# Kernel optimization log

Measured on AMD Instinct MI355X. Metric: run time of the kernel, lower is better.

Reference implementation:

```python
import jax, jax.numpy as jnp
import numpy as np

BATCH, DIM, L, N = 2, 768, 2048, 16


def setup_inputs() -> dict:
    key = jax.random.key(0)
    ks = jax.random.split(key, 8)
    u = jax.random.normal(ks[0], (BATCH, DIM, L), dtype=jnp.float32)
    delta = jax.random.uniform(ks[1], (BATCH, DIM, L), dtype=jnp.float32)
    # A must be negative for a stable SSM (exp(delta*A) <= 1)
    A = -jax.random.uniform(ks[2], (DIM, N), dtype=jnp.float32, minval=0.5, maxval=1.5)
    B = jax.random.normal(ks[3], (BATCH, N, L), dtype=jnp.float32)
    C = jax.random.normal(ks[4], (BATCH, N, L), dtype=jnp.float32)
    D = jax.random.normal(ks[5], (DIM,), dtype=jnp.float32)
    z = jax.random.normal(ks[6], (BATCH, DIM, L), dtype=jnp.float32)
    delta_bias = 0.1 * jax.random.normal(ks[7], (DIM,), dtype=jnp.float32)
    return {"u": u, "delta": delta, "A": A, "B": B, "C": C,
            "D": D, "z": z, "delta_bias": delta_bias}


def _selective_scan(u, delta, A, B, C, D, z, delta_bias):
    # delta_softplus=True path of mamba_ssm selective_scan_fn
    delta = jax.nn.softplus(delta + delta_bias[None, :, None])  # (b, d, l)
    # discretize: deltaA = exp(delta * A), deltaB_u = delta * B * u
    deltaA = jnp.exp(jnp.einsum('bdl,dn->lbdn', delta, A))          # (l, b, d, n)
    deltaBu = jnp.einsum('bdl,bnl,bdl->lbdn', delta, B, u)          # (l, b, d, n)
    C_t = jnp.transpose(C, (2, 0, 1))                               # (l, b, n)

    def step(x, inp):
        a, bu, c = inp
        x = a * x + bu                                              # (b, d, n)
        y = jnp.einsum('bdn,bn->bd', x, c)                          # (b, d)
        return x, y

    x0 = jnp.zeros((BATCH, DIM, N), dtype=u.dtype)
    _, ys = jax.lax.scan(step, x0, (deltaA, deltaBu, C_t))          # ys: (l, b, d)
    y = jnp.transpose(ys, (1, 2, 0))                                # (b, d, l)
    out = y + u * D[None, :, None]
    out = out * jax.nn.silu(z)
    return out


def reference(u, delta, A, B, C, D, z, delta_bias):
    return _selective_scan(u, delta, A, B, C, D, z, delta_bias)
```

## Files before the change

kernel.cpp:

```cpp
#include <hip/hip_runtime.h>


#define LOG2E 1.4426950408889634f
#define LN2   0.6931471805599453f

constexpr int BATCH = 2, DIM = 768, L = 2048, N = 16;
constexpr int NC = 64, LC = 32;
static_assert(NC * LC == L, "chunking must cover L");

__device__ __forceinline__ float fexp2(float x) {
#if __has_builtin(__builtin_amdgcn_exp2f)
  return __builtin_amdgcn_exp2f(x);
#else
  return exp2f(x);
#endif
}

__device__ __forceinline__ float frcp(float x) {
#if __has_builtin(__builtin_amdgcn_rcpf)
  return __builtin_amdgcn_rcpf(x);
#else
  return 1.0f / x;
#endif
}

__device__ __forceinline__ float softplus(float v) {
  float s = LN2 * __log2f(1.0f + fexp2(v * LOG2E));
  return (v > 20.0f) ? v : s;
}

__device__ __forceinline__ float silu(float v) {
  float e = fexp2(-v * LOG2E);
  return v * frcp(1.0f + e);
}

__global__ __launch_bounds__(256) void k_transpose(
    const float* __restrict__ Bm, const float* __restrict__ Cm,
    float* __restrict__ Bt, float* __restrict__ Ct) {
  int g = blockIdx.x * 256 + threadIdx.x;
  int l = g % L, b = g / L;
#pragma unroll
  for (int n = 0; n < N; n++) {
    Bt[((long)b * L + l) * N + n] = Bm[((long)b * N + n) * L + l];
    Ct[((long)b * L + l) * N + n] = Cm[((long)b * N + n) * L + l];
  }
}

__global__ __launch_bounds__(64) void k_pass1(
    const float* __restrict__ u, const float* __restrict__ delta,
    const float* __restrict__ A, const float* __restrict__ dbias,
    const float* __restrict__ Bt, float* __restrict__ h, float* __restrict__ P) {
  int bi = blockIdx.x;
  int c = bi / 24;
  int r = bi % 24;
  int b = r / 12;
  int dg = r % 12;
  int d = dg * 64 + threadIdx.x;

  float A2[N];
#pragma unroll
  for (int n = 0; n < N; n++) A2[n] = A[d * N + n] * LOG2E;
  float bias = dbias[d];

  float x[N];
#pragma unroll
  for (int n = 0; n < N; n++) x[n] = 0.0f;
  float S = 0.0f;

  long base = ((long)(b * DIM + d)) * L + c * LC;
  const float* Brow = Bt + ((long)b * L + c * LC) * N;

  for (int half = 0; half < 2; ++half) {
    float dl[16], uu[16];
#pragma unroll
    for (int j4 = 0; j4 < 4; j4++) {
      float4 dv = *(const float4*)(delta + base + half * 16 + j4 * 4);
      float4 uv = *(const float4*)(u + base + half * 16 + j4 * 4);
      dl[j4 * 4 + 0] = dv.x; dl[j4 * 4 + 1] = dv.y; dl[j4 * 4 + 2] = dv.z; dl[j4 * 4 + 3] = dv.w;
      uu[j4 * 4 + 0] = uv.x; uu[j4 * 4 + 1] = uv.y; uu[j4 * 4 + 2] = uv.z; uu[j4 * 4 + 3] = uv.w;
    }
#pragma unroll
    for (int j = 0; j < 16; j++) {
      float sp = softplus(dl[j] + bias);
      S += sp;
      float du = sp * uu[j];
      const float* br = Brow + (half * 16 + j) * N;
#pragma unroll
      for (int n = 0; n < N; n++) {
        float a = fexp2(sp * A2[n]);
        x[n] = a * x[n] + du * br[n];
      }
    }
  }

  long hb = ((long)(b * DIM + d) * NC + c) * N;
#pragma unroll
  for (int n = 0; n < N; n++) {
    h[hb + n] = x[n];
    P[hb + n] = fexp2(S * A2[n]);
  }
}

__global__ __launch_bounds__(256) void k_pass2(float* __restrict__ h, const float* __restrict__ P) {
  int t = blockIdx.x * 256 + threadIdx.x;
  int n = t % N;
  int bd = t / N;
  long base = (long)bd * NC * N + n;
  float x = 0.0f;
#pragma unroll 8
  for (int c = 0; c < NC; c++) {
    long i = base + (long)c * N;
    float Pc = P[i];
    float hc = h[i];
    h[i] = x;
    x = Pc * x + hc;
  }
}

__global__ __launch_bounds__(64) void k_pass3(
    const float* __restrict__ u, const float* __restrict__ delta,
    const float* __restrict__ A, const float* __restrict__ dbias,
    const float* __restrict__ Bt, const float* __restrict__ Ct,
    const float* __restrict__ Dv, const float* __restrict__ z,
    const float* __restrict__ xinit, float* __restrict__ out) {
  int bi = blockIdx.x;
  int c = bi / 24;
  int r = bi % 24;
  int b = r / 12;
  int dg = r % 12;
  int d = dg * 64 + threadIdx.x;

  float A2[N];
#pragma unroll
  for (int n = 0; n < N; n++) A2[n] = A[d * N + n] * LOG2E;
  float bias = dbias[d];
  float Dd = Dv[d];

  long hb = ((long)(b * DIM + d) * NC + c) * N;
  float x[N];
#pragma unroll
  for (int n = 0; n < N; n++) x[n] = xinit[hb + n];

  long base = ((long)(b * DIM + d)) * L + c * LC;
  const float* Brow = Bt + ((long)b * L + c * LC) * N;
  const float* Crow = Ct + ((long)b * L + c * LC) * N;

  for (int half = 0; half < 2; ++half) {
    float dl[16], uu[16], y[16];
#pragma unroll
    for (int j4 = 0; j4 < 4; j4++) {
      float4 dv = *(const float4*)(delta + base + half * 16 + j4 * 4);
      float4 uv = *(const float4*)(u + base + half * 16 + j4 * 4);
      dl[j4 * 4 + 0] = dv.x; dl[j4 * 4 + 1] = dv.y; dl[j4 * 4 + 2] = dv.z; dl[j4 * 4 + 3] = dv.w;
      uu[j4 * 4 + 0] = uv.x; uu[j4 * 4 + 1] = uv.y; uu[j4 * 4 + 2] = uv.z; uu[j4 * 4 + 3] = uv.w;
    }
#pragma unroll
    for (int j = 0; j < 16; j++) {
      float sp = softplus(dl[j] + bias);
      float du = sp * uu[j];
      const float* br = Brow + (half * 16 + j) * N;
      const float* cr = Crow + (half * 16 + j) * N;
      float acc = 0.0f;
#pragma unroll
      for (int n = 0; n < N; n++) {
        float a = fexp2(sp * A2[n]);
        x[n] = a * x[n] + du * br[n];
        acc += x[n] * cr[n];
      }
      y[j] = acc;
    }
#pragma unroll
    for (int j4 = 0; j4 < 4; j4++) {
      float4 zv = *(const float4*)(z + base + half * 16 + j4 * 4);
      float4 ov;
      ov.x = (y[j4 * 4 + 0] + uu[j4 * 4 + 0] * Dd) * silu(zv.x);
      ov.y = (y[j4 * 4 + 1] + uu[j4 * 4 + 1] * Dd) * silu(zv.y);
      ov.z = (y[j4 * 4 + 2] + uu[j4 * 4 + 2] * Dd) * silu(zv.z);
      ov.w = (y[j4 * 4 + 3] + uu[j4 * 4 + 3] * Dd) * silu(zv.w);
      *(float4*)(out + base + half * 16 + j4 * 4) = ov;
    }
  }
}

__global__ __launch_bounds__(256) void k_simple(
    const float* __restrict__ u, const float* __restrict__ delta,
    const float* __restrict__ A, const float* __restrict__ dbias,
    const float* __restrict__ Bm, const float* __restrict__ Cm,
    const float* __restrict__ Dv, const float* __restrict__ z,
    float* __restrict__ out) {
  int t = blockIdx.x * 256 + threadIdx.x;
  int n = t % N;
  int bd = t / N;
  int d = bd % DIM;
  int b = bd / DIM;
  float A2 = A[d * N + n] * LOG2E;
  float bias = dbias[d];
  float Dd = Dv[d];
  const float* Bp = Bm + ((long)b * N + n) * L;
  const float* Cp = Cm + ((long)b * N + n) * L;
  long base = (long)bd * L;
  float x = 0.0f;
  for (int l = 0; l < L; l++) {
    float dv = delta[base + l];
    float uv = u[base + l];
    float sp = softplus(dv + bias);
    float a = fexp2(sp * A2);
    x = a * x + sp * uv * Bp[l];
    float y = x * Cp[l];
#pragma unroll
    for (int off = 8; off; off >>= 1) y += __shfl_xor(y, off, 16);
    if (n == 0) {
      float zv = z[base + l];
      out[base + l] = (y + uv * Dd) * silu(zv);
    }
  }
}

extern "C" void kernel_launch(void* const* d_in, const int* in_sizes, int n_in,
                              void* d_out, int out_size, void* d_ws, size_t ws_size,
                              hipStream_t stream) {
  const float* u     = (const float*)d_in[0];
  const float* delta = (const float*)d_in[1];
  const float* A     = (const float*)d_in[2];
  const float* Bm    = (const float*)d_in[3];
  const float* Cm    = (const float*)d_in[4];
  const float* Dv    = (const float*)d_in[5];
  const float* z     = (const float*)d_in[6];
  const float* dbias = (const float*)d_in[7];
  float* out = (float*)d_out;

  const size_t btct = (size_t)BATCH * L * N;
  const size_t hp   = (size_t)BATCH * DIM * NC * N;
  const size_t need = (2 * btct + 2 * hp) * sizeof(float);

  if (ws_size < need) {
    k_simple<<<(BATCH * DIM * N) / 256, 256, 0, stream>>>(u, delta, A, dbias, Bm, Cm, Dv, z, out);
    return;
  }

  float* ws = (float*)d_ws;
  float* Bt = ws;
  float* Ct = Bt + btct;
  float* h  = Ct + btct;
  float* P  = h + hp;

  k_transpose<<<(BATCH * L) / 256, 256, 0, stream>>>(Bm, Cm, Bt, Ct);
  k_pass1<<<NC * 24, 64, 0, stream>>>(u, delta, A, dbias, Bt, h, P);
  k_pass2<<<(BATCH * DIM * N) / 256, 256, 0, stream>>>(h, P);
  k_pass3<<<NC * 24, 64, 0, stream>>>(u, delta, A, dbias, Bt, Ct, Dv, z, h, out);
}
```

Measured before the change: 147.3 us.

## Stage B/C tiles in shared memory, drop transpose kernel, halve chunk length

Removes the separate B/C transpose kernel. Each 256-thread block (four waves, four chunks) now loads its B and C tiles straight from the original layout into LDS. Chunk length drops from 32 to 16 with twice as many chunks, giving more parallel blocks. The chunk decay factor P is no longer stored: only the softplus sum is kept and pass2 recomputes the exp. The h layout is reordered so pass1 and pass3 can use float4 stores and loads. The cost is a longer serial chain in pass2 (128 chunks) and a larger h workspace.

```diff
diff --git a/kernel.cpp b/kernel.cpp
--- a/kernel.cpp
+++ b/kernel.cpp
@@ -5,24 +5,13 @@
 #define LN2   0.6931471805599453f
 
 constexpr int BATCH = 2, DIM = 768, L = 2048, N = 16;
-constexpr int NC = 64, LC = 32;
+constexpr int NC = 128, LC = 16;
+constexpr int DG = DIM / 64;
+constexpr int CPB = 4;
+constexpr int CG = NC / CPB;
 static_assert(NC * LC == L, "chunking must cover L");
 
-__device__ __forceinline__ float fexp2(float x) {
-#if __has_builtin(__builtin_amdgcn_exp2f)
-  return __builtin_amdgcn_exp2f(x);
-#else
-  return exp2f(x);
-#endif
-}
-
-__device__ __forceinline__ float frcp(float x) {
-#if __has_builtin(__builtin_amdgcn_rcpf)
-  return __builtin_amdgcn_rcpf(x);
-#else
-  return 1.0f / x;
-#endif
-}
+__device__ __forceinline__ float fexp2(float x) { return __builtin_amdgcn_exp2f(x); }
 
 __device__ __forceinline__ float softplus(float v) {
   float s = LN2 * __log2f(1.0f + fexp2(v * LOG2E));
@@ -30,155 +19,188 @@
 }
 
 __device__ __forceinline__ float silu(float v) {
-  float e = fexp2(-v * LOG2E);
-  return v * frcp(1.0f + e);
-}
-
-__global__ __launch_bounds__(256) void k_transpose(
-    const float* __restrict__ Bm, const float* __restrict__ Cm,
-    float* __restrict__ Bt, float* __restrict__ Ct) {
-  int g = blockIdx.x * 256 + threadIdx.x;
-  int l = g % L, b = g / L;
-#pragma unroll
-  for (int n = 0; n < N; n++) {
-    Bt[((long)b * L + l) * N + n] = Bm[((long)b * N + n) * L + l];
-    Ct[((long)b * L + l) * N + n] = Cm[((long)b * N + n) * L + l];
-  }
-}
-
-__global__ __launch_bounds__(64) void k_pass1(
+  return v / (1.0f + fexp2(-v * LOG2E));
+}
+
+__global__ __launch_bounds__(256) void k_pass1(
     const float* __restrict__ u, const float* __restrict__ delta,
     const float* __restrict__ A, const float* __restrict__ dbias,
-    const float* __restrict__ Bt, float* __restrict__ h, float* __restrict__ P) {
-  int bi = blockIdx.x;
-  int c = bi / 24;
-  int r = bi % 24;
-  int b = r / 12;
-  int dg = r % 12;
-  int d = dg * 64 + threadIdx.x;
+    const float* __restrict__ Bg, float* __restrict__ h, float* __restrict__ Ssum) {
+  __shared__ float Bs[N][CPB * LC + 4];
+  int blk = blockIdx.x;
+  int cg = blk % CG;
+  int r = blk / CG;
+  int dg = r % DG;
+  int b = r / DG;
+  int t = threadIdx.x;
+
+  {
+    int n = t >> 4, jj = t & 15;
+    const float* src = Bg + ((long)(b * N + n)) * L + cg * (CPB * LC) + jj * 4;
+    float4 v = *(const float4*)src;
+    Bs[n][jj * 4 + 0] = v.x; Bs[n][jj * 4 + 1] = v.y;
+    Bs[n][jj * 4 + 2] = v.z; Bs[n][jj * 4 + 3] = v.w;
+  }
+
+  int wave = t >> 6, lane = t & 63;
+  int c = cg * CPB + wave;
+  int d = dg * 64 + lane;
 
   float A2[N];
 #pragma unroll
-  for (int n = 0; n < N; n++) A2[n] = A[d * N + n] * LOG2E;
+  for (int q = 0; q < 4; q++) {
+    float4 av = *(const float4*)(A + d * N + q * 4);
+    A2[q * 4 + 0] = av.x * LOG2E; A2[q * 4 + 1] = av.y * LOG2E;
+    A2[q * 4 + 2] = av.z * LOG2E; A2[q * 4 + 3] = av.w * LOG2E;
+  }
   float bias = dbias[d];
 
+  long base = ((long)(b * DIM + d)) * L + c * LC;
+  float dl[LC], uu[LC];
+#pragma unroll
+  for (int j4 = 0; j4 < 4; j4++) {
+    float4 dv = *(const float4*)(delta + base + j4 * 4);
+    float4 uv = *(const float4*)(u + base + j4 * 4);
+    dl[j4 * 4 + 0] = dv.x; dl[j4 * 4 + 1] = dv.y; dl[j4 * 4 + 2] = dv.z; dl[j4 * 4 + 3] = dv.w;
+    uu[j4 * 4 + 0] = uv.x; uu[j4 * 4 + 1] = uv.y; uu[j4 * 4 + 2] = uv.z; uu[j4 * 4 + 3] = uv.w;
+  }
+
+  float sp[LC], S = 0.0f;
+#pragma unroll
+  for (int j = 0; j < LC; j++) { sp[j] = softplus(dl[j] + bias); S += sp[j]; }
+
+  __syncthreads();
+
   float x[N];
 #pragma unroll
   for (int n = 0; n < N; n++) x[n] = 0.0f;
-  float S = 0.0f;
-
-  long base = ((long)(b * DIM + d)) * L + c * LC;
-  const float* Brow = Bt + ((long)b * L + c * LC) * N;
-
-  for (int half = 0; half < 2; ++half) {
-    float dl[16], uu[16];
-#pragma unroll
-    for (int j4 = 0; j4 < 4; j4++) {
-      float4 dv = *(const float4*)(delta + base + half * 16 + j4 * 4);
-      float4 uv = *(const float4*)(u + base + half * 16 + j4 * 4);
-      dl[j4 * 4 + 0] = dv.x; dl[j4 * 4 + 1] = dv.y; dl[j4 * 4 + 2] = dv.z; dl[j4 * 4 + 3] = dv.w;
-      uu[j4 * 4 + 0] = uv.x; uu[j4 * 4 + 1] = uv.y; uu[j4 * 4 + 2] = uv.z; uu[j4 * 4 + 3] = uv.w;
+  int col0 = wave * LC;
+#pragma unroll
+  for (int j = 0; j < LC; j++) {
+    float du = sp[j] * uu[j];
+#pragma unroll
+    for (int n = 0; n < N; n++) {
+      float a = fexp2(sp[j] * A2[n]);
+      x[n] = a * x[n] + du * Bs[n][col0 + j];
     }
-#pragma unroll
-    for (int j = 0; j < 16; j++) {
-      float sp = softplus(dl[j] + bias);
-      S += sp;
-      float du = sp * uu[j];
-      const float* br = Brow + (half * 16 + j) * N;
-#pragma unroll
-      for (int n = 0; n < N; n++) {
-        float a = fexp2(sp * A2[n]);
-        x[n] = a * x[n] + du * br[n];
-      }
-    }
-  }
-
-  long hb = ((long)(b * DIM + d) * NC + c) * N;
-#pragma unroll
-  for (int n = 0; n < N; n++) {
-    h[hb + n] = x[n];
-    P[hb + n] = fexp2(S * A2[n]);
-  }
-}
-
-__global__ __launch_bounds__(256) void k_pass2(float* __restrict__ h, const float* __restrict__ P) {
-  int t = blockIdx.x * 256 + threadIdx.x;
-  int n = t % N;
-  int bd = t / N;
-  long base = (long)bd * NC * N + n;
+  }
+
+  long hb = ((long)((b * NC + c) * DIM + d)) * N;
+#pragma unroll
+  for (int q = 0; q < 4; q++) {
+    float4 v; v.x = x[q * 4 + 0]; v.y = x[q * 4 + 1]; v.z = x[q * 4 + 2]; v.w = x[q * 4 + 3];
+    *(float4*)(h + hb + q * 4) = v;
+  }
+  Ssum[(b * NC + c) * DIM + d] = S;
+}
+
+__global__ __launch_bounds__(256) void k_pass2(
+    float* __restrict__ h, const float* __restrict__ Ssum, const float* __restrict__ A) {
+  int g = blockIdx.x * 256 + threadIdx.x;
+  int n = g & 15;
+  int d = (g >> 4) % DIM;
+  int b = g / (16 * DIM);
+  float A2 = A[d * N + n] * LOG2E;
   float x = 0.0f;
-#pragma unroll 8
+#pragma unroll 4
   for (int c = 0; c < NC; c++) {
-    long i = base + (long)c * N;
-    float Pc = P[i];
-    float hc = h[i];
-    h[i] = x;
-    x = Pc * x + hc;
-  }
-}
-
-__global__ __launch_bounds__(64) void k_pass3(
+    long idx = ((long)((b * NC + c) * DIM + d)) * N + n;
+    float hc = h[idx];
+    float Sc = Ssum[(b * NC + c) * DIM + d];
+    float xi = x;
+    x = fexp2(Sc * A2) * x + hc;
+    h[idx] = xi;
+  }
+}
+
+__global__ __launch_bounds__(256) void k_pass3(
     const float* __restrict__ u, const float* __restrict__ delta,
     const float* __restrict__ A, const float* __restrict__ dbias,
-    const float* __restrict__ Bt, const float* __restrict__ Ct,
+    const float* __restrict__ Bg, const float* __restrict__ Cg,
     const float* __restrict__ Dv, const float* __restrict__ z,
     const float* __restrict__ xinit, float* __restrict__ out) {
-  int bi = blockIdx.x;
-  int c = bi / 24;
-  int r = bi % 24;
-  int b = r / 12;
-  int dg = r % 12;
-  int d = dg * 64 + threadIdx.x;
+  __shared__ float Bs[N][CPB * LC + 4];
+  __shared__ float Cs[N][CPB * LC + 4];
+  int blk = blockIdx.x;
+  int cg = blk % CG;
+  int r = blk / CG;
+  int dg = r % DG;
+  int b = r / DG;
+  int t = threadIdx.x;
+
+  {
+    int n = t >> 4, jj = t & 15;
+    long off = ((long)(b * N + n)) * L + cg * (CPB * LC) + jj * 4;
+    float4 v = *(const float4*)(Bg + off);
+    Bs[n][jj * 4 + 0] = v.x; Bs[n][jj * 4 + 1] = v.y;
+    Bs[n][jj * 4 + 2] = v.z; Bs[n][jj * 4 + 3] = v.w;
+    float4 w = *(const float4*)(Cg + off);
+    Cs[n][jj * 4 + 0] = w.x; Cs[n][jj * 4 + 1] = w.y;
+    Cs[n][jj * 4 + 2] = w.z; Cs[n][jj * 4 + 3] = w.w;
+  }
+
+  int wave = t >> 6, lane = t & 63;
+  int c = cg * CPB + wave;
+  int d = dg * 64 + lane;
 
   float A2[N];
 #pragma unroll
-  for (int n = 0; n < N; n++) A2[n] = A[d * N + n] * LOG2E;
+  for (int q = 0; q < 4; q++) {
+    float4 av = *(const float4*)(A + d * N + q * 4);
+    A2[q * 4 + 0] = av.x * LOG2E; A2[q * 4 + 1] = av.y * LOG2E;
+    A2[q * 4 + 2] = av.z * LOG2E; A2[q * 4 + 3] = av.w * LOG2E;
+  }
   float bias = dbias[d];
   float Dd = Dv[d];
 
-  long hb = ((long)(b * DIM + d) * NC + c) * N;
+  long hb = ((long)((b * NC + c) * DIM + d)) * N;
   float x[N];
 #pragma unroll
-  for (int n = 0; n < N; n++) x[n] = xinit[hb + n];
+  for (int q = 0; q < 4; q++) {
+    float4 v = *(const float4*)(xinit + hb + q * 4);
+    x[q * 4 + 0] = v.x; x[q * 4 + 1] = v.y; x[q * 4 + 2] = v.z; x[q * 4 + 3] = v.w;
+  }
 
   long base = ((long)(b * DIM + d)) * L + c * LC;
-  const float* Brow = Bt + ((long)b * L + c * LC) * N;
-  const float* Crow = Ct + ((long)b * L + c * LC) * N;
-
-  for (int half = 0; half < 2; ++half) {
-    float dl[16], uu[16], y[16];
-#pragma unroll
-    for (int j4 = 0; j4 < 4; j4++) {
-      float4 dv = *(const float4*)(delta + base + half * 16 + j4 * 4);
-      float4 uv = *(const float4*)(u + base + half * 16 + j4 * 4);
-      dl[j4 * 4 + 0] = dv.x; dl[j4 * 4 + 1] = dv.y; dl[j4 * 4 + 2] = dv.z; dl[j4 * 4 + 3] = dv.w;
-      uu[j4 * 4 + 0] = uv.x; uu[j4 * 4 + 1] = uv.y; uu[j4 * 4 + 2] = uv.z; uu[j4 * 4 + 3] = uv.w;
+  float dl[LC], uu[LC];
+#pragma unroll
+  for (int j4 = 0; j4 < 4; j4++) {
+    float4 dv = *(const float4*)(delta + base + j4 * 4);
+    float4 uv = *(const float4*)(u + base + j4 * 4);
+    dl[j4 * 4 + 0] = dv.x; dl[j4 * 4 + 1] = dv.y; dl[j4 * 4 + 2] = dv.z; dl[j4 * 4 + 3] = dv.w;
+    uu[j4 * 4 + 0] = uv.x; uu[j4 * 4 + 1] = uv.y; uu[j4 * 4 + 2] = uv.z; uu[j4 * 4 + 3] = uv.w;
+  }
+
+  float sp[LC];
+#pragma unroll
+  for (int j = 0; j < LC; j++) sp[j] = softplus(dl[j] + bias);
+
+  __syncthreads();
+
+  float y[LC];
+  int col0 = wave * LC;
+#pragma unroll
+  for (int j = 0; j < LC; j++) {
+    float du = sp[j] * uu[j];
+    float acc = 0.0f;
+#pragma unroll
+    for (int n = 0; n < N; n++) {
+      float a = fexp2(sp[j] * A2[n]);
+      x[n] = a * x[n] + du * Bs[n][col0 + j];
+      acc += x[n] * Cs[n][col0 + j];
     }
-#pragma unroll
-    for (int j = 0; j < 16; j++) {
-      float sp = softplus(dl[j] + bias);
-      float du = sp * uu[j];
-      const float* br = Brow + (half * 16 + j) * N;
-      const float* cr = Crow + (half * 16 + j) * N;
-      float acc = 0.0f;
-#pragma unroll
-      for (int n = 0; n < N; n++) {
-        float a = fexp2(sp * A2[n]);
-        x[n] = a * x[n] + du * br[n];
-        acc += x[n] * cr[n];
-      }
-      y[j] = acc;
-    }
-#pragma unroll
-    for (int j4 = 0; j4 < 4; j4++) {
-      float4 zv = *(const float4*)(z + base + half * 16 + j4 * 4);
-      float4 ov;
-      ov.x = (y[j4 * 4 + 0] + uu[j4 * 4 + 0] * Dd) * silu(zv.x);
-      ov.y = (y[j4 * 4 + 1] + uu[j4 * 4 + 1] * Dd) * silu(zv.y);
-      ov.z = (y[j4 * 4 + 2] + uu[j4 * 4 + 2] * Dd) * silu(zv.z);
-      ov.w = (y[j4 * 4 + 3] + uu[j4 * 4 + 3] * Dd) * silu(zv.w);
-      *(float4*)(out + base + half * 16 + j4 * 4) = ov;
-    }
+    y[j] = acc;
+  }
+
+#pragma unroll
+  for (int j4 = 0; j4 < 4; j4++) {
+    float4 zv = *(const float4*)(z + base + j4 * 4);
+    float4 ov;
+    ov.x = (y[j4 * 4 + 0] + uu[j4 * 4 + 0] * Dd) * silu(zv.x);
+    ov.y = (y[j4 * 4 + 1] + uu[j4 * 4 + 1] * Dd) * silu(zv.y);
+    ov.z = (y[j4 * 4 + 2] + uu[j4 * 4 + 2] * Dd) * silu(zv.z);
+    ov.w = (y[j4 * 4 + 3] + uu[j4 * 4 + 3] * Dd) * silu(zv.w);
+    *(float4*)(out + base + j4 * 4) = ov;
   }
 }
 
@@ -229,23 +251,20 @@
   const float* dbias = (const float*)d_in[7];
   float* out = (float*)d_out;
 
-  const size_t btct = (size_t)BATCH * L * N;
-  const size_t hp   = (size_t)BATCH * DIM * NC * N;
-  const size_t need = (2 * btct + 2 * hp) * sizeof(float);
+  const size_t hp = (size_t)BATCH * NC * DIM * N;
+  const size_t sp = (size_t)BATCH * NC * DIM;
+  const size_t need = (hp + sp) * sizeof(float);
 
   if (ws_size < need) {
     k_simple<<<(BATCH * DIM * N) / 256, 256, 0, stream>>>(u, delta, A, dbias, Bm, Cm, Dv, z, out);
     return;
   }
 
-  float* ws = (float*)d_ws;
-  float* Bt = ws;
-  float* Ct = Bt + btct;
-  float* h  = Ct + btct;
-  float* P  = h + hp;
-
-  k_transpose<<<(BATCH * L) / 256, 256, 0, stream>>>(Bm, Cm, Bt, Ct);
-  k_pass1<<<NC * 24, 64, 0, stream>>>(u, delta, A, dbias, Bt, h, P);
-  k_pass2<<<(BATCH * DIM * N) / 256, 256, 0, stream>>>(h, P);
-  k_pass3<<<NC * 24, 64, 0, stream>>>(u, delta, A, dbias, Bt, Ct, Dv, z, h, out);
-}
+  float* h = (float*)d_ws;
+  float* S = h + hp;
+
+  const int grid13 = BATCH * DG * CG;
+  k_pass1<<<grid13, 256, 0, stream>>>(u, delta, A, dbias, Bm, h, S);
+  k_pass2<<<(BATCH * DIM * N) / 256, 256, 0, stream>>>(h, S, A);
+  k_pass3<<<grid13, 256, 0, stream>>>(u, delta, A, dbias, Bm, Cm, Dv, z, h, out);
+}
```

Result: faster. 140.9 us (-4.3%).
